# Performance work log

Measured on AMD Instinct MI355X. Metric: run time of the kernel, lower is better.

Reference implementation:

```python
import jax, jax.numpy as jnp
import numpy as np

B, S, H = 4, 1024, 256      # batch, num_spans, hidden
R = 65536                   # num_relations
FFN = int(2 * H * 1.5)      # 768


def setup_inputs() -> dict:
    key = jax.random.key(0)
    k1, k2, k3, k4 = jax.random.split(key, 4)
    span_reps = jax.random.normal(k1, (B, S, H), dtype=jnp.float32)
    rel_ids = jax.random.randint(k2, (B, R, 2), 0, S, dtype=jnp.int64)
    W1 = jax.random.normal(k3, (2 * H, FFN), dtype=jnp.float32) * (1.0 / np.sqrt(2 * H))
    b1 = jnp.zeros((FFN,), dtype=jnp.float32)
    W2 = jax.random.normal(k4, (FFN, H), dtype=jnp.float32) * (1.0 / np.sqrt(FFN))
    b2 = jnp.zeros((H,), dtype=jnp.float32)
    return {"span_reps": span_reps, "rel_ids": rel_ids, "W1": W1, "b1": b1, "W2": W2, "b2": b2}


def reference(span_reps, rel_ids, W1, b1, W2, b2):
    # gather head/tail span reps: (B, R, H) each
    head = jnp.take_along_axis(span_reps, rel_ids[..., 0:1], axis=1)  # via batched gather
    tail = jnp.take_along_axis(span_reps, rel_ids[..., 1:2], axis=1)
    rel = jnp.concatenate([head, tail], axis=-1)  # (B, R, 2H)
    # FFN projection: Linear -> ReLU -> (dropout: identity at eval) -> Linear
    h = jax.nn.relu(jnp.einsum('brk,kf->brf', rel, W1) + b1)
    out = jnp.einsum('brf,fh->brh', h, W2) + b2  # (B, R, H)
    return out
```

## Files before the change

### kernel.cpp

```cpp
#include <hip/hip_runtime.h>

#define NB 4
#define NS 1024
#define NH 256
#define NR 65536
#define NF 768
#define NK 512

typedef __attribute__((ext_vector_type(8))) short bf16x8;
typedef __attribute__((ext_vector_type(4))) float f32x4;

static __device__ __forceinline__ unsigned short f2bf(float f) {
  unsigned int u = __builtin_bit_cast(unsigned int, f);
  u += 0x7FFFu + ((u >> 16) & 1u);
  return (unsigned short)(u >> 16);
}

static __device__ __forceinline__ unsigned cvt_pk(float a, float b) {
  unsigned r;
  asm("v_cvt_pk_bf16_f32 %0, %1, %2" : "=v"(r) : "v"(a), "v"(b));
  return r;
}

#define BARRIER()                                            \
  do {                                                       \
    asm volatile("s_waitcnt lgkmcnt(0)" ::: "memory");       \
    __builtin_amdgcn_s_barrier();                            \
    asm volatile("" ::: "memory");                           \
  } while (0)

__global__ void prep_all(const float* __restrict__ w1, const float* __restrict__ w2,
                         const int* __restrict__ ids,
                         unsigned short* __restrict__ w1f,
                         unsigned short* __restrict__ w2f,
                         int* __restrict__ flag) {
  int bid = blockIdx.x;
  if (bid < 192) {
    int t = bid * 256 + threadIdx.x;
    int l = t & 63;
    int kk = (t >> 6) & 15;
    int half = (t >> 10) & 1;
    int w = (t >> 11) & 3;
    int c = t >> 13;
    int row = c * 128 + w * 32 + half * 16 + (l & 15);
    int k0 = kk * 32 + (l >> 4) * 8;
    uint4 pk;
    unsigned short v[8];
#pragma unroll
    for (int j = 0; j < 8; ++j) v[j] = f2bf(w1[(size_t)(k0 + j) * NF + row]);
    pk.x = v[0] | ((unsigned)v[1] << 16);
    pk.y = v[2] | ((unsigned)v[3] << 16);
    pk.z = v[4] | ((unsigned)v[5] << 16);
    pk.w = v[6] | ((unsigned)v[7] << 16);
    *(uint4*)(w1f + (size_t)t * 8) = pk;
  } else if (bid < 288) {
    int t = (bid - 192) * 256 + threadIdx.x;
    int l = t & 63;
    int kq = (t >> 6) & 3;
    int rest = t >> 8;
    int c = rest % 6;
    int wn = rest / 6;
    int nj = wn & 3;
    int w = wn >> 2;
    int row = w * 64 + nj * 16 + (l & 15);
    int k = c * 128 + kq * 32 + (l >> 4) * 8;
    uint4 pk;
    unsigned short v[8];
#pragma unroll
    for (int j = 0; j < 8; ++j) v[j] = f2bf(w2[(size_t)(k + j) * NH + row]);
    pk.x = v[0] | ((unsigned)v[1] << 16);
    pk.y = v[2] | ((unsigned)v[3] << 16);
    pk.z = v[4] | ((unsigned)v[5] << 16);
    pk.w = v[6] | ((unsigned)v[7] << 16);
    *(uint4*)(w2f + (size_t)t * 8) = pk;
  } else {
    __shared__ int anynz;
    if (threadIdx.x == 0) anynz = 0;
    __syncthreads();
    int acc = 0;
    for (int i = threadIdx.x; i < 8192; i += 256) acc |= ids[2 * i + 1];
    if (acc != 0) atomicOr(&anynz, 1);
    __syncthreads();
    if (threadIdx.x == 0) flag[0] = (anynz == 0) ? 1 : 0;
  }
}

__global__ __launch_bounds__(256, 2)
void fused_relffn(const float* __restrict__ span, const int* __restrict__ ids,
                  const float* __restrict__ b1, const float* __restrict__ b2,
                  const unsigned short* __restrict__ w1f,
                  const unsigned short* __restrict__ w2f,
                  const int* __restrict__ flagp, float* __restrict__ out) {
  __shared__ __align__(16) unsigned short As[64 * 512];
  __shared__ __align__(16) unsigned short Hs[64 * 128];

  const int tid = threadIdx.x;
  const int blk = blockIdx.x;
  const int bb = blk >> 10;
  const int r0 = (blk & 1023) << 6;
  const int lane = tid & 63;
  const int w = tid >> 6;
  const int l15 = lane & 15;
  const int lq = lane >> 4;
  const int is64 = flagp[0];
  const int rot = blk % 3;

  const unsigned short* w1base = w1f + w * 16384 + lane * 8;
  const unsigned short* w2base = w2f + w * 49152 + lane * 8;

  bf16x8 wfa[2][2], wfb[2][2];
  {
    const unsigned short* wpa0 = w1base + (rot * 2) * 65536;
    const unsigned short* wpb0 = w1base + (rot * 2 + 1) * 65536;
#pragma unroll
    for (int d = 0; d < 2; ++d) {
      wfa[d][0] = *(const bf16x8*)(wpa0 + d * 512);
      wfa[d][1] = *(const bf16x8*)(wpa0 + 8192 + d * 512);
      wfb[d][0] = *(const bf16x8*)(wpb0 + d * 512);
      wfb[d][1] = *(const bf16x8*)(wpb0 + 8192 + d * 512);
    }
  }

  {
    const long pair0 = ((long)bb * NR + r0) * 2;
    int idv[16];
#pragma unroll
    for (int j = 0; j < 16; ++j) {
      int g = tid + j * 256;
      int row = g >> 6;
      int kc = g & 63;
      long pidx = pair0 + row * 2 + (kc >> 5);
      idv[j] = is64 ? ids[pidx * 2] : ids[pidx];
    }
#pragma unroll
    for (int j = 0; j < 16; ++j) {
      int g = tid + j * 256;
      int row = g >> 6;
      int kc = g & 63;
      const float* src = span + ((size_t)bb * NS + idv[j]) * NH + (kc & 31) * 8;
      float4 v0 = *(const float4*)src;
      float4 v1 = *(const float4*)(src + 4);
      uint4 pk;
      pk.x = cvt_pk(v0.x, v0.y);
      pk.y = cvt_pk(v0.z, v0.w);
      pk.z = cvt_pk(v1.x, v1.y);
      pk.w = cvt_pk(v1.z, v1.w);
      int idx = row * 512 + ((kc * 8) ^ ((row & 7) << 3));
      *(uint4*)&As[idx] = pk;
    }
  }
  BARRIER();

  f32x4 acc2[4][4];
#pragma unroll
  for (int mi = 0; mi < 4; ++mi)
#pragma unroll
    for (int nj = 0; nj < 4; ++nj) {
      f32x4 z = {0.f, 0.f, 0.f, 0.f};
      acc2[mi][nj] = z;
    }

  for (int cpi = 0; cpi < 3; ++cpi) {
    const int cp = (cpi + rot) % 3;
    const int ca = cp * 2, cb = ca + 1;
    const unsigned short* wpa = w1base + ca * 65536;
    const unsigned short* wpb = w1base + cb * 65536;

    f32x4 acc1a[4][2], acc1b[4][2];
#pragma unroll
    for (int mi = 0; mi < 4; ++mi)
#pragma unroll
      for (int ni = 0; ni < 2; ++ni) {
        f32x4 z = {0.f, 0.f, 0.f, 0.f};
        acc1a[mi][ni] = z;
        acc1b[mi][ni] = z;
      }

    bf16x8 afp[2][4];
#pragma unroll
    for (int mi = 0; mi < 4; ++mi) {
      int row = mi * 16 + l15;
      afp[0][mi] = *(const bf16x8*)&As[row * 512 + ((lq * 8) ^ ((row & 7) << 3))];
    }

#pragma unroll
    for (int kk = 0; kk < 16; ++kk) {
      const int cur = kk & 1;
      if (kk < 15) {
#pragma unroll
        for (int mi = 0; mi < 4; ++mi) {
          int row = mi * 16 + l15;
          int kidx = (kk + 1) * 32 + lq * 8;
          afp[cur ^ 1][mi] = *(const bf16x8*)&As[row * 512 + (kidx ^ ((row & 7) << 3))];
        }
      }
      bf16x8 ca0 = wfa[cur][0], ca1 = wfa[cur][1];
      bf16x8 cb0 = wfb[cur][0], cb1 = wfb[cur][1];
      if (kk < 14) {
        wfa[cur][0] = *(const bf16x8*)(wpa + (kk + 2) * 512);
        wfa[cur][1] = *(const bf16x8*)(wpa + 8192 + (kk + 2) * 512);
        wfb[cur][0] = *(const bf16x8*)(wpb + (kk + 2) * 512);
        wfb[cur][1] = *(const bf16x8*)(wpb + 8192 + (kk + 2) * 512);
      }
      __builtin_amdgcn_s_setprio(1);
#pragma unroll
      for (int mi = 0; mi < 4; ++mi) {
        bf16x8 a = afp[cur][mi];
        acc1a[mi][0] = __builtin_amdgcn_mfma_f32_16x16x32_bf16(ca0, a, acc1a[mi][0], 0, 0, 0);
        acc1a[mi][1] = __builtin_amdgcn_mfma_f32_16x16x32_bf16(ca1, a, acc1a[mi][1], 0, 0, 0);
        acc1b[mi][0] = __builtin_amdgcn_mfma_f32_16x16x32_bf16(cb0, a, acc1b[mi][0], 0, 0, 0);
        acc1b[mi][1] = __builtin_amdgcn_mfma_f32_16x16x32_bf16(cb1, a, acc1b[mi][1], 0, 0, 0);
      }
      __builtin_amdgcn_s_setprio(0);
    }

    if (cpi < 2) {
      const int cpn = (cpi + 1 + rot) % 3;
      const unsigned short* npa = w1base + (cpn * 2) * 65536;
      const unsigned short* npb = w1base + (cpn * 2 + 1) * 65536;
#pragma unroll
      for (int d = 0; d < 2; ++d) {
        wfa[d][0] = *(const bf16x8*)(npa + d * 512);
        wfa[d][1] = *(const bf16x8*)(npa + 8192 + d * 512);
        wfb[d][0] = *(const bf16x8*)(npb + d * 512);
        wfb[d][1] = *(const bf16x8*)(npb + 8192 + d * 512);
      }
    }

#pragma unroll
    for (int half = 0; half < 2; ++half) {
      const int c = half ? cb : ca;
      BARRIER();
#pragma unroll
      for (int ni = 0; ni < 2; ++ni) {
        int n0 = c * 128 + w * 32 + ni * 16 + lq * 4;
        float4 bv = *(const float4*)(b1 + n0);
#pragma unroll
        for (int mi = 0; mi < 4; ++mi) {
          f32x4 a = half ? acc1b[mi][ni] : acc1a[mi][ni];
          float x0 = fmaxf(a[0] + bv.x, 0.0f);
          float x1 = fmaxf(a[1] + bv.y, 0.0f);
          float x2 = fmaxf(a[2] + bv.z, 0.0f);
          float x3 = fmaxf(a[3] + bv.w, 0.0f);
          int m = mi * 16 + l15;
          int nl0 = w * 32 + ni * 16 + lq * 4;
          uint2 pk;
          pk.x = cvt_pk(x0, x1);
          pk.y = cvt_pk(x2, x3);
          *(uint2*)&Hs[m * 128 + (nl0 ^ ((m & 7) << 3))] = pk;
        }
      }
      BARRIER();
      const unsigned short* w2p = w2base + c * 2048;
#pragma unroll
      for (int kq = 0; kq < 4; ++kq) {
        bf16x8 vf[4];
#pragma unroll
        for (int nj = 0; nj < 4; ++nj)
          vf[nj] = *(const bf16x8*)(w2p + nj * 12288 + kq * 512);
        bf16x8 hf[4];
#pragma unroll
        for (int mi = 0; mi < 4; ++mi) {
          int row = mi * 16 + l15;
          int kidx = kq * 32 + lq * 8;
          hf[mi] = *(const bf16x8*)&Hs[row * 128 + (kidx ^ ((row & 7) << 3))];
        }
        __builtin_amdgcn_s_setprio(1);
#pragma unroll
        for (int mi = 0; mi < 4; ++mi)
#pragma unroll
          for (int nj = 0; nj < 4; ++nj)
            acc2[mi][nj] = __builtin_amdgcn_mfma_f32_16x16x32_bf16(vf[nj], hf[mi], acc2[mi][nj], 0, 0, 0);
        __builtin_amdgcn_s_setprio(0);
      }
    }
  }

#pragma unroll
  for (int nj = 0; nj < 4; ++nj) {
    int n0 = w * 64 + nj * 16 + lq * 4;
    float4 bv = *(const float4*)(b2 + n0);
#pragma unroll
    for (int mi = 0; mi < 4; ++mi) {
      int m = mi * 16 + l15;
      f32x4 a = acc2[mi][nj];
      float4 o;
      o.x = a[0] + bv.x; o.y = a[1] + bv.y; o.z = a[2] + bv.z; o.w = a[3] + bv.w;
      *(float4*)(out + ((size_t)bb * NR + r0 + m) * NH + n0) = o;
    }
  }
}

extern "C" void kernel_launch(void* const* d_in, const int* in_sizes, int n_in,
                              void* d_out, int out_size, void* d_ws, size_t ws_size,
                              hipStream_t stream) {
  const float* span = (const float*)d_in[0];
  const int* ids = (const int*)d_in[1];
  const float* W1 = (const float*)d_in[2];
  const float* b1 = (const float*)d_in[3];
  const float* W2 = (const float*)d_in[4];
  const float* b2 = (const float*)d_in[5];
  float* out = (float*)d_out;

  char* ws = (char*)d_ws;
  int* flag = (int*)ws;
  unsigned short* w1f = (unsigned short*)(ws + 64);
  unsigned short* w2f = (unsigned short*)(ws + 64 + NF * NK * 2);

  prep_all<<<289, 256, 0, stream>>>(W1, W2, ids, w1f, w2f, flag);
  fused_relffn<<<4096, 256, 0, stream>>>(span, ids, b1, b2, w1f, w2f, flag, out);
}
```

Before: 305.7 us.

## Split fused relation FFN into two kernels staging hidden activations in workspace

Splits the fused gather+FFN kernel into a first-GEMM kernel that writes bf16 ReLU activations to a global workspace and a second-GEMM kernel that reads them back. The passes are chosen by workspace size, and the old fused kernel remains as the fallback. The aim is to relieve register and LDS pressure and raise occupancy for the second GEMM. The cost is a large extra round trip of the hidden activations through global memory.

```diff
diff --git a/kernel.cpp b/kernel.cpp
--- a/kernel.cpp
+++ b/kernel.cpp
@@ -86,39 +86,33 @@
 }
 
 __global__ __launch_bounds__(256, 2)
-void fused_relffn(const float* __restrict__ span, const int* __restrict__ ids,
-                  const float* __restrict__ b1, const float* __restrict__ b2,
-                  const unsigned short* __restrict__ w1f,
-                  const unsigned short* __restrict__ w2f,
-                  const int* __restrict__ flagp, float* __restrict__ out) {
+void g1_kernel(const float* __restrict__ span, const int* __restrict__ ids,
+               const float* __restrict__ b1,
+               const unsigned short* __restrict__ w1f,
+               const int* __restrict__ flagp,
+               unsigned short* __restrict__ h, int bb0) {
   __shared__ __align__(16) unsigned short As[64 * 512];
-  __shared__ __align__(16) unsigned short Hs[64 * 128];
 
   const int tid = threadIdx.x;
   const int blk = blockIdx.x;
-  const int bb = blk >> 10;
+  const int bb = bb0 + (blk >> 10);
   const int r0 = (blk & 1023) << 6;
   const int lane = tid & 63;
   const int w = tid >> 6;
   const int l15 = lane & 15;
   const int lq = lane >> 4;
   const int is64 = flagp[0];
-  const int rot = blk % 3;
 
   const unsigned short* w1base = w1f + w * 16384 + lane * 8;
-  const unsigned short* w2base = w2f + w * 49152 + lane * 8;
+  unsigned short* htile = h + (size_t)blk * 49152;
 
   bf16x8 wfa[2][2], wfb[2][2];
-  {
-    const unsigned short* wpa0 = w1base + (rot * 2) * 65536;
-    const unsigned short* wpb0 = w1base + (rot * 2 + 1) * 65536;
-#pragma unroll
-    for (int d = 0; d < 2; ++d) {
-      wfa[d][0] = *(const bf16x8*)(wpa0 + d * 512);
-      wfa[d][1] = *(const bf16x8*)(wpa0 + 8192 + d * 512);
-      wfb[d][0] = *(const bf16x8*)(wpb0 + d * 512);
-      wfb[d][1] = *(const bf16x8*)(wpb0 + 8192 + d * 512);
-    }
+#pragma unroll
+  for (int d = 0; d < 2; ++d) {
+    wfa[d][0] = *(const bf16x8*)(w1base + d * 512);
+    wfa[d][1] = *(const bf16x8*)(w1base + 8192 + d * 512);
+    wfb[d][0] = *(const bf16x8*)(w1base + 65536 + d * 512);
+    wfb[d][1] = *(const bf16x8*)(w1base + 65536 + 8192 + d * 512);
   }
 
   {
@@ -151,6 +145,251 @@
   }
   BARRIER();
 
+  for (int cp = 0; cp < 3; ++cp) {
+    const int ca = cp * 2, cb = ca + 1;
+    const unsigned short* wpa = w1base + ca * 65536;
+    const unsigned short* wpb = w1base + cb * 65536;
+
+    f32x4 acc1a[4][2], acc1b[4][2];
+#pragma unroll
+    for (int mi = 0; mi < 4; ++mi)
+#pragma unroll
+      for (int ni = 0; ni < 2; ++ni) {
+        f32x4 z = {0.f, 0.f, 0.f, 0.f};
+        acc1a[mi][ni] = z;
+        acc1b[mi][ni] = z;
+      }
+
+    bf16x8 afp[2][4];
+#pragma unroll
+    for (int mi = 0; mi < 4; ++mi) {
+      int row = mi * 16 + l15;
+      afp[0][mi] = *(const bf16x8*)&As[row * 512 + ((lq * 8) ^ ((row & 7) << 3))];
+    }
+
+#pragma unroll
+    for (int kk = 0; kk < 16; ++kk) {
+      const int cur = kk & 1;
+      if (kk < 15) {
+#pragma unroll
+        for (int mi = 0; mi < 4; ++mi) {
+          int row = mi * 16 + l15;
+          int kidx = (kk + 1) * 32 + lq * 8;
+          afp[cur ^ 1][mi] = *(const bf16x8*)&As[row * 512 + (kidx ^ ((row & 7) << 3))];
+        }
+      }
+      bf16x8 ca0 = wfa[cur][0], ca1 = wfa[cur][1];
+      bf16x8 cb0 = wfb[cur][0], cb1 = wfb[cur][1];
+      if (kk < 14) {
+        wfa[cur][0] = *(const bf16x8*)(wpa + (kk + 2) * 512);
+        wfa[cur][1] = *(const bf16x8*)(wpa + 8192 + (kk + 2) * 512);
+        wfb[cur][0] = *(const bf16x8*)(wpb + (kk + 2) * 512);
+        wfb[cur][1] = *(const bf16x8*)(wpb + 8192 + (kk + 2) * 512);
+      }
+      __builtin_amdgcn_s_setprio(1);
+#pragma unroll
+      for (int mi = 0; mi < 4; ++mi) {
+        bf16x8 a = afp[cur][mi];
+        acc1a[mi][0] = __builtin_amdgcn_mfma_f32_16x16x32_bf16(ca0, a, acc1a[mi][0], 0, 0, 0);
+        acc1a[mi][1] = __builtin_amdgcn_mfma_f32_16x16x32_bf16(ca1, a, acc1a[mi][1], 0, 0, 0);
+        acc1b[mi][0] = __builtin_amdgcn_mfma_f32_16x16x32_bf16(cb0, a, acc1b[mi][0], 0, 0, 0);
+        acc1b[mi][1] = __builtin_amdgcn_mfma_f32_16x16x32_bf16(cb1, a, acc1b[mi][1], 0, 0, 0);
+      }
+      __builtin_amdgcn_s_setprio(0);
+    }
+
+    if (cp < 2) {
+      const unsigned short* npa = w1base + (ca + 2) * 65536;
+      const unsigned short* npb = w1base + (cb + 2) * 65536;
+#pragma unroll
+      for (int d = 0; d < 2; ++d) {
+        wfa[d][0] = *(const bf16x8*)(npa + d * 512);
+        wfa[d][1] = *(const bf16x8*)(npa + 8192 + d * 512);
+        wfb[d][0] = *(const bf16x8*)(npb + d * 512);
+        wfb[d][1] = *(const bf16x8*)(npb + 8192 + d * 512);
+      }
+    }
+
+#pragma unroll
+    for (int half = 0; half < 2; ++half) {
+      const int c = half ? cb : ca;
+      const int ubase = ((c * 4 + w) * 4) << 9;
+#pragma unroll
+      for (int ni = 0; ni < 2; ++ni) {
+        int n0 = c * 128 + w * 32 + ni * 16 + lq * 4;
+        float4 bv = *(const float4*)(b1 + n0);
+#pragma unroll
+        for (int mi = 0; mi < 4; ++mi) {
+          f32x4 a = half ? acc1b[mi][ni] : acc1a[mi][ni];
+          float x0 = fmaxf(a[0] + bv.x, 0.0f);
+          float x1 = fmaxf(a[1] + bv.y, 0.0f);
+          float x2 = fmaxf(a[2] + bv.z, 0.0f);
+          float x3 = fmaxf(a[3] + bv.w, 0.0f);
+          uint2 pk;
+          pk.x = cvt_pk(x0, x1);
+          pk.y = cvt_pk(x2, x3);
+          int off = ubase + (mi << 9) +
+                    ((l15 + 32 * ni + 16 * (lq >> 1)) << 3) + ((lq & 1) << 2);
+          *(uint2*)&htile[off] = pk;
+        }
+      }
+    }
+  }
+}
+
+__global__ __launch_bounds__(256, 3)
+void g2_kernel(const unsigned short* __restrict__ h,
+               const unsigned short* __restrict__ w2f,
+               const float* __restrict__ b2, float* __restrict__ out, int bb0) {
+  __shared__ __align__(16) unsigned short hb[2][8192];
+
+  const int tid = threadIdx.x;
+  const int blk = blockIdx.x;
+  const int bb = bb0 + (blk >> 10);
+  const int r0 = (blk & 1023) << 6;
+  const int lane = tid & 63;
+  const int w = tid >> 6;
+  const int l15 = lane & 15;
+  const int lq = lane >> 4;
+
+  const unsigned short* hbase = h + (size_t)blk * 49152;
+  const unsigned short* w2base = w2f + w * 49152 + lane * 8;
+
+  f32x4 acc2[4][4];
+#pragma unroll
+  for (int mi = 0; mi < 4; ++mi)
+#pragma unroll
+    for (int nj = 0; nj < 4; ++nj) {
+      f32x4 z = {0.f, 0.f, 0.f, 0.f};
+      acc2[mi][nj] = z;
+    }
+
+  uint4 st[4];
+#pragma unroll
+  for (int j = 0; j < 4; ++j)
+    st[j] = *(const uint4*)&hbase[(w * 4 + j) * 512 + lane * 8];
+#pragma unroll
+  for (int j = 0; j < 4; ++j)
+    *(uint4*)&hb[0][(w * 4 + j) * 512 + lane * 8] = st[j];
+  __syncthreads();
+
+  int cur = 0;
+  for (int g = 0; g < 6; ++g) {
+    if (g < 5) {
+      const unsigned short* src = hbase + (g + 1) * 8192;
+#pragma unroll
+      for (int j = 0; j < 4; ++j)
+        st[j] = *(const uint4*)&src[(w * 4 + j) * 512 + lane * 8];
+    }
+#pragma unroll
+    for (int kqL = 0; kqL < 4; ++kqL) {
+      const int kq = g * 4 + kqL;
+      bf16x8 vf[4];
+#pragma unroll
+      for (int nj = 0; nj < 4; ++nj)
+        vf[nj] = *(const bf16x8*)(w2base + nj * 12288 + (kq >> 2) * 2048 + (kq & 3) * 512);
+      bf16x8 hf[4];
+#pragma unroll
+      for (int mi = 0; mi < 4; ++mi)
+        hf[mi] = *(const bf16x8*)&hb[cur][(kqL * 4 + mi) * 512 + lane * 8];
+      __builtin_amdgcn_s_setprio(1);
+#pragma unroll
+      for (int mi = 0; mi < 4; ++mi)
+#pragma unroll
+        for (int nj = 0; nj < 4; ++nj)
+          acc2[mi][nj] = __builtin_amdgcn_mfma_f32_16x16x32_bf16(vf[nj], hf[mi], acc2[mi][nj], 0, 0, 0);
+      __builtin_amdgcn_s_setprio(0);
+    }
+    __syncthreads();
+    if (g < 5) {
+#pragma unroll
+      for (int j = 0; j < 4; ++j)
+        *(uint4*)&hb[cur ^ 1][(w * 4 + j) * 512 + lane * 8] = st[j];
+    }
+    __syncthreads();
+    cur ^= 1;
+  }
+
+#pragma unroll
+  for (int nj = 0; nj < 4; ++nj) {
+    int n0 = w * 64 + nj * 16 + lq * 4;
+    float4 bv = *(const float4*)(b2 + n0);
+#pragma unroll
+    for (int mi = 0; mi < 4; ++mi) {
+      int m = mi * 16 + l15;
+      f32x4 a = acc2[mi][nj];
+      float4 o;
+      o.x = a[0] + bv.x; o.y = a[1] + bv.y; o.z = a[2] + bv.z; o.w = a[3] + bv.w;
+      *(float4*)(out + ((size_t)bb * NR + r0 + m) * NH + n0) = o;
+    }
+  }
+}
+
+__global__ __launch_bounds__(256, 2)
+void fused_relffn(const float* __restrict__ span, const int* __restrict__ ids,
+                  const float* __restrict__ b1, const float* __restrict__ b2,
+                  const unsigned short* __restrict__ w1f,
+                  const unsigned short* __restrict__ w2f,
+                  const int* __restrict__ flagp, float* __restrict__ out) {
+  __shared__ __align__(16) unsigned short As[64 * 512];
+  __shared__ __align__(16) unsigned short Hs[64 * 128];
+
+  const int tid = threadIdx.x;
+  const int blk = blockIdx.x;
+  const int bb = blk >> 10;
+  const int r0 = (blk & 1023) << 6;
+  const int lane = tid & 63;
+  const int w = tid >> 6;
+  const int l15 = lane & 15;
+  const int lq = lane >> 4;
+  const int is64 = flagp[0];
+  const int rot = blk % 3;
+
+  const unsigned short* w1base = w1f + w * 16384 + lane * 8;
+  const unsigned short* w2base = w2f + w * 49152 + lane * 8;
+
+  bf16x8 wfa[2][2], wfb[2][2];
+  {
+    const unsigned short* wpa0 = w1base + (rot * 2) * 65536;
+    const unsigned short* wpb0 = w1base + (rot * 2 + 1) * 65536;
+#pragma unroll
+    for (int d = 0; d < 2; ++d) {
+      wfa[d][0] = *(const bf16x8*)(wpa0 + d * 512);
+      wfa[d][1] = *(const bf16x8*)(wpa0 + 8192 + d * 512);
+      wfb[d][0] = *(const bf16x8*)(wpb0 + d * 512);
+      wfb[d][1] = *(const bf16x8*)(wpb0 + 8192 + d * 512);
+    }
+  }
+  {
+    const long pair0 = ((long)bb * NR + r0) * 2;
+    int idv[16];
+#pragma unroll
+    for (int j = 0; j < 16; ++j) {
+      int g = tid + j * 256;
+      int row = g >> 6;
+      int kc = g & 63;
+      long pidx = pair0 + row * 2 + (kc >> 5);
+      idv[j] = is64 ? ids[pidx * 2] : ids[pidx];
+    }
+#pragma unroll
+    for (int j = 0; j < 16; ++j) {
+      int g = tid + j * 256;
+      int row = g >> 6;
+      int kc = g & 63;
+      const float* src = span + ((size_t)bb * NS + idv[j]) * NH + (kc & 31) * 8;
+      float4 v0 = *(const float4*)src;
+      float4 v1 = *(const float4*)(src + 4);
+      uint4 pk;
+      pk.x = cvt_pk(v0.x, v0.y);
+      pk.y = cvt_pk(v0.z, v0.w);
+      pk.z = cvt_pk(v1.x, v1.y);
+      pk.w = cvt_pk(v1.z, v1.w);
+      int idx = row * 512 + ((kc * 8) ^ ((row & 7) << 3));
+      *(uint4*)&As[idx] = pk;
+    }
+  }
+  BARRIER();
+
   f32x4 acc2[4][4];
 #pragma unroll
   for (int mi = 0; mi < 4; ++mi)
@@ -305,8 +544,25 @@
   char* ws = (char*)d_ws;
   int* flag = (int*)ws;
   unsigned short* w1f = (unsigned short*)(ws + 64);
-  unsigned short* w2f = (unsigned short*)(ws + 64 + NF * NK * 2);
+  unsigned short* w2f = (unsigned short*)(ws + 64 + 786432);
+  const size_t off_h = ((64 + 786432 + 393216 + 255) / 256) * 256;
+  unsigned short* hws = (unsigned short*)(ws + off_h);
+  const size_t per_batch = (size_t)1024 * 49152 * 2;
 
   prep_all<<<289, 256, 0, stream>>>(W1, W2, ids, w1f, w2f, flag);
-  fused_relffn<<<4096, 256, 0, stream>>>(span, ids, b1, b2, w1f, w2f, flag, out);
-}
+
+  int g = 0;
+  if (ws_size >= off_h + 4 * per_batch) g = 4;
+  else if (ws_size >= off_h + 2 * per_batch) g = 2;
+  else if (ws_size >= off_h + 1 * per_batch) g = 1;
+
+  if (g == 0) {
+    fused_relffn<<<4096, 256, 0, stream>>>(span, ids, b1, b2, w1f, w2f, flag, out);
+  } else {
+    const int npass = 4 / g;
+    for (int p = 0; p < npass; ++p) {
+      g1_kernel<<<g * 1024, 256, 0, stream>>>(span, ids, b1, w1f, flag, hws, p * g);
+      g2_kernel<<<g * 1024, 256, 0, stream>>>(hws, w2f, b2, out, p * g);
+    }
+  }
+}
```

Result: slower. 896.8 us (+193.4%).
